# Kernel tuning notes

Measured on AMD Instinct MI355X. Metric: run time of the kernel, lower is better.

Reference implementation:

```python
import jax, jax.numpy as jnp
import numpy as np

L, D, H, F = 2, 512, 8, 2048
B, S = 1, 2048
DH = D // H
EPS = 1e-6
NEG = -1e9


def setup_inputs() -> dict:
    key = jax.random.key(0)
    ks = jax.random.split(key, 8)
    s = 0.02
    return {
        "x": jax.random.normal(ks[0], (B, S, D), jnp.float32),
        "enc_output": jax.random.normal(ks[1], (B, S, D), jnp.float32),
        # per-layer stacked params; axis 1 of attn weights = [wq, wk, wv, wo]
        "attn1_w": jax.random.normal(ks[2], (L, 4, D, D), jnp.float32) * s,
        "attn1_b": jnp.zeros((L, 4, D), jnp.float32),
        "attn2_w": jax.random.normal(ks[3], (L, 4, D, D), jnp.float32) * s,
        "attn2_b": jnp.zeros((L, 4, D), jnp.float32),
        "ffn_w1": jax.random.normal(ks[4], (L, D, F), jnp.float32) * s,
        "ffn_b1": jnp.zeros((L, F), jnp.float32),
        "ffn_w2": jax.random.normal(ks[5], (L, F, D), jnp.float32) * s,
        "ffn_b2": jnp.zeros((L, D), jnp.float32),
        # axis 1 = [norm1, norm2, norm3]
        "ln_g": jnp.ones((L, 3, D), jnp.float32),
        "ln_b": jnp.zeros((L, 3, D), jnp.float32),
    }


def positional_encoding(seq_len, num_feat):
    pos = jnp.arange(seq_len, dtype=jnp.float32)[:, None]
    dims = jnp.arange(num_feat, dtype=jnp.float32)[None, :]
    rates = 1.0 / jnp.power(10000.0, 2.0 * jnp.floor(dims / 2.0) / num_feat)
    ang = pos * rates  # [S, D]
    # keras module concatenates sines(even cols) and cosines(odd cols)
    return jnp.concatenate([jnp.sin(ang[:, 0::2]), jnp.cos(ang[:, 1::2])], axis=-1)[None]


def layer_norm(x, g, b):
    mu = jnp.mean(x, axis=-1, keepdims=True)
    var = jnp.mean(jnp.square(x - mu), axis=-1, keepdims=True)
    return (x - mu) * jax.lax.rsqrt(var + EPS) * g + b


def split_heads(x):
    b, s, _ = x.shape
    return x.reshape(b, s, H, DH).transpose(0, 2, 1, 3)  # [B,H,S,dh]


def mha(q_in, k_in, v_in, w, bias, mask):
    q = split_heads(q_in @ w[0] + bias[0])
    k = split_heads(k_in @ w[1] + bias[1])
    v = split_heads(v_in @ w[2] + bias[2])
    logits = jnp.einsum("bhqd,bhkd->bhqk", q, k) / jnp.sqrt(jnp.float32(DH))
    if mask is not None:
        logits = logits + mask * NEG
    weights = jax.nn.softmax(logits, axis=-1)
    out = jnp.einsum("bhqk,bhkd->bhqd", weights, v)
    b, _, s, _ = out.shape
    out = out.transpose(0, 2, 1, 3).reshape(b, s, D)
    return out @ w[3] + bias[3]


def decoder_forward(x, enc_output, attn1_w, attn1_b, attn2_w, attn2_b,
                    ffn_w1, ffn_b1, ffn_w2, ffn_b2, ln_g, ln_b):
    s = x.shape[1]
    x = x + positional_encoding(s, x.shape[2])
    causal = jnp.triu(jnp.ones((s, s), jnp.float32), k=1)[None, None]  # 1 = masked

    def layer(x, p):
        a1w, a1b, a2w, a2b, w1, b1, w2, b2, g, bn = p
        attn1 = mha(x, x, x, a1w, a1b, causal)
        x = layer_norm(x + attn1, g[0], bn[0])
        attn2 = mha(x, enc_output, enc_output, a2w, a2b, None)
        x = layer_norm(x + attn2, g[1], bn[1])
        ffn = jax.nn.relu(x @ w1 + b1) @ w2 + b2
        x = layer_norm(x + ffn, g[2], bn[2])
        return x, None

    x, _ = jax.lax.scan(layer, x, (attn1_w, attn1_b, attn2_w, attn2_b,
                                   ffn_w1, ffn_b1, ffn_w2, ffn_b2, ln_g, ln_b))
    return x


def reference(x, enc_output, attn1_w, attn1_b, attn2_w, attn2_b,
              ffn_w1, ffn_b1, ffn_w2, ffn_b2, ln_g, ln_b):
    return decoder_forward(x, enc_output, attn1_w, attn1_b, attn2_w, attn2_b,
                           ffn_w1, ffn_b1, ffn_w2, ffn_b2, ln_g, ln_b)
```

## Files before the change

### kernel.cpp

```cpp
#include <hip/hip_runtime.h>
#include <hip/hip_bf16.h>
#include <math.h>

#define S 2048
#define D 512
#define H 8
#define DH 64
#define F 2048
#define NLAYER 2

typedef __attribute__((ext_vector_type(8))) short bf16x8;
typedef __attribute__((ext_vector_type(4))) float f32x4;
typedef __hip_bfloat16 bf16;

typedef __attribute__((address_space(3))) unsigned int lds_u32;
typedef __attribute__((address_space(1))) const unsigned int glb_u32;

__device__ __forceinline__ void gld16(const void* g, void* l) {
    __builtin_amdgcn_global_load_lds((glb_u32*)g, (lds_u32*)l, 16, 0, 0);
}

__global__ void prep_kernel(const float* __restrict__ x, const float* __restrict__ enc,
                            float* __restrict__ xbF, bf16* __restrict__ xbB,
                            bf16* __restrict__ encB) {
    int idx = blockIdx.x * blockDim.x + threadIdx.x;
    if (idx >= S * D) return;
    int s = idx / D;
    int j = idx % D;
    int jj = (j < D / 2) ? j : j - D / 2;
    float rate = expf(-(float)jj * (logf(10000.0f) / (float)(D / 2)));
    float ang = (float)s * rate;
    float pe = (j < D / 2) ? sinf(ang) : cosf(ang);
    float v = x[idx] + pe;
    xbF[idx] = v;
    xbB[idx] = __float2bfloat16(v);
    encB[idx] = __float2bfloat16(enc[idx]);
}

__global__ __launch_bounds__(256)
void transpose_cvt_b(const float* __restrict__ in, bf16* __restrict__ out, int R, int C,
                     size_t inStride, size_t outL, size_t outM, int mpl)
{
    __shared__ float t[64][65];
    const int z = blockIdx.z;
    const float* src = in + (size_t)z * inStride;
    bf16* dst = out + (size_t)(z / mpl) * outL + (size_t)(z % mpl) * outM;
    const int rb = blockIdx.x * 64, cb = blockIdx.y * 64;
    for (int i = threadIdx.x; i < 4096; i += 256) {
        int r = i >> 6, c = i & 63;
        t[r][c] = src[(size_t)(rb + r) * C + cb + c];
    }
    __syncthreads();
    for (int i = threadIdx.x; i < 4096; i += 256) {
        int r = i >> 6, c = i & 63;
        dst[(size_t)(cb + r) * R + rb + c] = __float2bfloat16(t[c][r]);
    }
}

template<int BM, int BN, int BK, int MODE>
__global__ __launch_bounds__(256)
void gemm_bf16(const bf16* __restrict__ A, const bf16* __restrict__ Bt,
               const float* __restrict__ bias, float* __restrict__ outF,
               bf16* __restrict__ outB, int K, int ldc, int relu,
               bf16* __restrict__ q16, bf16* __restrict__ kh,
               bf16* __restrict__ vt, int qn, int kn)
{
    constexpr int MI = BM / 32, NJ = BN / 32;
    constexpr int SL = BK / 8;
    constexpr int KS = BK / 32;
    constexpr int HALF = (BM + BN) * BK * 2;
    constexpr int IA = BM * SL / 256, IB = BN * SL / 256;
    __shared__ char lds[2 * HALF];
    const int tid = threadIdx.x;
    const int w = tid >> 6, l = tid & 63;
    const int l15 = l & 15, l4 = l >> 4;
    const int bm = blockIdx.y * BM, bn = blockIdx.x * BN;
    const int wr = (w >> 1) * (BM / 2), wc = (w & 1) * (BN / 2);

    f32x4 acc[MI][NJ] = {};

#define XV(row) ((BK == 64) ? ((row) & 7) : (((row) >> 1) & 3))
#define GSTAGE(k0, b)                                                          \
    {                                                                          \
        _Pragma("unroll")                                                      \
        for (int i = 0; i < IA; ++i) {                                         \
            int n = (w * IA + i) * 64 + l;                                     \
            int row = n / SL;                                                  \
            int sl = (n % SL) ^ XV(row);                                       \
            gld16(A + (size_t)(bm + row) * K + (k0) + sl * 8,                  \
                  lds + (b) * HALF + (w * IA + i) * 1024);                     \
        }                                                                      \
        _Pragma("unroll")                                                      \
        for (int i = 0; i < IB; ++i) {                                         \
            int n = (w * IB + i) * 64 + l;                                     \
            int row = n / SL;                                                  \
            int sl = (n % SL) ^ XV(row);                                       \
            gld16(Bt + (size_t)(bn + row) * K + (k0) + sl * 8,                 \
                  lds + (b) * HALF + BM * BK * 2 + (w * IB + i) * 1024);       \
        }                                                                      \
    }

    GSTAGE(0, 0);
    __syncthreads();
    int cur = 0;
    for (int k0 = 0; k0 < K; k0 += BK) {
        if (k0 + BK < K) GSTAGE(k0 + BK, cur ^ 1);
        const char* base = lds + cur * HALF;
        bf16x8 af[MI][KS], bfr[NJ][KS];
#pragma unroll
        for (int i = 0; i < MI; ++i) {
            int row = wr + i * 16 + l15;
#pragma unroll
            for (int s = 0; s < KS; ++s)
                af[i][s] = *(const bf16x8*)(base + row * (BK * 2)
                                            + (((s * 4 + l4) ^ XV(row)) << 4));
        }
#pragma unroll
        for (int j = 0; j < NJ; ++j) {
            int row = wc + j * 16 + l15;
#pragma unroll
            for (int s = 0; s < KS; ++s)
                bfr[j][s] = *(const bf16x8*)(base + BM * BK * 2 + row * (BK * 2)
                                             + (((s * 4 + l4) ^ XV(row)) << 4));
        }
#pragma unroll
        for (int s = 0; s < KS; ++s)
#pragma unroll
            for (int i = 0; i < MI; ++i)
#pragma unroll
                for (int j = 0; j < NJ; ++j)
                    acc[i][j] = __builtin_amdgcn_mfma_f32_16x16x32_bf16(af[i][s], bfr[j][s], acc[i][j], 0, 0, 0);
        __syncthreads();
        cur ^= 1;
    }
#undef GSTAGE
#undef XV

    if (MODE == 0) {
#pragma unroll
        for (int i = 0; i < MI; ++i)
#pragma unroll
            for (int j = 0; j < NJ; ++j)
#pragma unroll
                for (int q = 0; q < 4; ++q) {
                    int row = bm + wr + i * 16 + l4 * 4 + q;
                    int col = bn + wc + j * 16 + l15;
                    float v = acc[i][j][q] + bias[col];
                    if (relu) v = fmaxf(v, 0.f);
                    if (outF) outF[(size_t)row * ldc + col] = v;
                    if (outB) outB[(size_t)row * ldc + col] = __float2bfloat16(v);
                }
    } else {
        const int creg = (bn < qn) ? 0 : (bn < qn + kn ? 1 : 2);
        if (creg < 2) {
#pragma unroll
            for (int i = 0; i < MI; ++i)
#pragma unroll
                for (int j = 0; j < NJ; ++j)
#pragma unroll
                    for (int q = 0; q < 4; ++q) {
                        int row = bm + wr + i * 16 + l4 * 4 + q;
                        int col = bn + wc + j * 16 + l15;
                        float v = acc[i][j][q] + bias[col];
                        if (creg == 0) {
                            q16[(size_t)row * 512 + col] = __float2bfloat16(v);
                        } else {
                            int c2 = col - qn;
                            kh[((size_t)(c2 >> 6) * S + row) * 64 + (c2 & 63)] = __float2bfloat16(v);
                        }
                    }
        } else {
            short* t = (short*)lds;
#pragma unroll
            for (int i = 0; i < MI; ++i)
#pragma unroll
                for (int j = 0; j < NJ; ++j)
#pragma unroll
                    for (int q = 0; q < 4; ++q) {
                        int r = wr + i * 16 + l4 * 4 + q;
                        int c = wc + j * 16 + l15;
                        float v = acc[i][j][q] + bias[bn + c];
                        t[r * 72 + c] = __builtin_bit_cast(short, __float2bfloat16(v));
                    }
            __syncthreads();
            const int dgb = bn - qn - kn;
            for (int i2 = tid; i2 < 512; i2 += 256) {
                int dl = i2 >> 3, s8 = (i2 & 7) * 8;
                bf16x8 v;
#pragma unroll
                for (int jj = 0; jj < 8; ++jj)
                    v[jj] = t[(s8 + jj) * 72 + dl];
                *(bf16x8*)(vt + (size_t)(dgb + dl) * S + bm + s8) = v;
            }
        }
    }
}

template<int CAUSAL>
__global__ __launch_bounds__(256)
void attn_mfma6(const bf16* __restrict__ Q, const bf16* __restrict__ Kh,
                const bf16* __restrict__ Vt, bf16* __restrict__ O)
{
    __shared__ char lds[40960];
    const int tid = threadIdx.x;
    const int w = tid >> 6, l = tid & 63;
    const int l15 = l & 15, l4 = l >> 4;
    const int h = blockIdx.x, qb = blockIdx.y;
    const int qw = qb * 64 + w * 16;
    const int qr = qw + l15;
    char* plds = lds + 32768 + w * 2048;

    const float QSC = 0.1803368801f;
    bf16x8 aq[2];
#pragma unroll
    for (int s = 0; s < 2; ++s) {
        bf16x8 raw = *(const bf16x8*)(Q + (size_t)(qw + l15) * 512 + h * DH + s * 32 + l4 * 8);
#pragma unroll
        for (int j = 0; j < 8; ++j) {
            float f = __builtin_bit_cast(float, ((unsigned int)(unsigned short)raw[j]) << 16) * QSC;
            raw[j] = __builtin_bit_cast(short, __float2bfloat16(f));
        }
        aq[s] = raw;
    }

    f32x4 o[4] = {};
    float mrun = -1e30f, lrun = 0.f;
    const int cmax = CAUSAL ? qb : (S / 64 - 1);

#define STAGE(c, b)                                                                 \
    {                                                                               \
        const int kb2 = (c) * 64;                                                   \
        _Pragma("unroll")                                                           \
        for (int i = 0; i < 2; ++i) {                                               \
            int n = w * 128 + i * 64 + l;                                           \
            int row = n >> 3;                                                       \
            int sl = (n & 7) ^ (row & 7);                                           \
            gld16(Kh + ((size_t)h * S + kb2 + row) * 64 + sl * 8,                   \
                  lds + (b) * 16384 + w * 2048 + i * 1024);                         \
            gld16(Vt + ((size_t)(h * 64 + row)) * S + kb2 + sl * 8,                 \
                  lds + (b) * 16384 + 8192 + w * 2048 + i * 1024);                  \
        }                                                                           \
    }

    STAGE(0, 0);
    __syncthreads();

    int cur = 0;
    for (int c = 0; c <= cmax; ++c) {
        if (c < cmax) STAGE(c + 1, cur ^ 1);
        const char* kb = lds + cur * 16384;
        const char* vb = kb + 8192;
        const int kbase = c * 64;

        f32x4 st[4];
#pragma unroll
        for (int t = 0; t < 4; ++t) {
            f32x4 sacc = {0.f, 0.f, 0.f, 0.f};
#pragma unroll
            for (int s = 0; s < 2; ++s) {
                bf16x8 kf = *(const bf16x8*)(kb + (t * 16 + l15) * 128
                                             + (((s * 4 + l4) ^ (l15 & 7)) << 4));
                sacc = __builtin_amdgcn_mfma_f32_16x16x32_bf16(kf, aq[s], sacc, 0, 0, 0);
            }
            st[t] = sacc;
        }

        float mx = -1e30f;
#pragma unroll
        for (int t = 0; t < 4; ++t)
#pragma unroll
            for (int r = 0; r < 4; ++r) {
                float v = st[t][r];
                if (CAUSAL && c == cmax) {
                    int key = kbase + t * 16 + l4 * 4 + r;
                    if (key > qr) v = -1e30f;
                }
                st[t][r] = v;
                mx = fmaxf(mx, v);
            }
        mx = fmaxf(mx, __shfl_xor(mx, 16));
        mx = fmaxf(mx, __shfl_xor(mx, 32));

        if (__any(mx > mrun + 8.0f)) {
            float mnew = fmaxf(mrun, mx);
            float scl = exp2f(mrun - mnew);
            mrun = mnew;
            lrun *= scl;
#pragma unroll
            for (int j = 0; j < 4; ++j) {
                float sj = __shfl(scl, (l & 48) | (l4 * 4 + j));
#pragma unroll
                for (int dt = 0; dt < 4; ++dt) o[dt][j] *= sj;
            }
        }

        float ps = 0.f;
#pragma unroll
        for (int t = 0; t < 4; ++t) {
            float e0 = exp2f(st[t][0] - mrun);
            float e1 = exp2f(st[t][1] - mrun);
            float e2 = exp2f(st[t][2] - mrun);
            float e3 = exp2f(st[t][3] - mrun);
            ps += (e0 + e1) + (e2 + e3);
            unsigned int lo = (unsigned int)(unsigned short)__builtin_bit_cast(short, __float2bfloat16(e0))
                            | ((unsigned int)(unsigned short)__builtin_bit_cast(short, __float2bfloat16(e1)) << 16);
            unsigned int hi = (unsigned int)(unsigned short)__builtin_bit_cast(short, __float2bfloat16(e2))
                            | ((unsigned int)(unsigned short)__builtin_bit_cast(short, __float2bfloat16(e3)) << 16);
            uint2 pk; pk.x = lo; pk.y = hi;
            int byte = (l15 * 128 + t * 32 + l4 * 8) ^ ((l15 & 7) << 4);
            *(uint2*)(plds + byte) = pk;
        }
        ps += __shfl_xor(ps, 16);
        ps += __shfl_xor(ps, 32);
        lrun += ps;

        bf16x8 pf[2];
#pragma unroll
        for (int s = 0; s < 2; ++s) {
            int byte = (l15 * 128 + s * 64 + l4 * 16) ^ ((l15 & 7) << 4);
            pf[s] = *(const bf16x8*)(plds + byte);
        }
#pragma unroll
        for (int dt = 0; dt < 4; ++dt)
#pragma unroll
            for (int s = 0; s < 2; ++s) {
                bf16x8 vf = *(const bf16x8*)(vb + (dt * 16 + l15) * 128
                                             + (((s * 4 + l4) ^ (l15 & 7)) << 4));
                o[dt] = __builtin_amdgcn_mfma_f32_16x16x32_bf16(pf[s], vf, o[dt], 0, 0, 0);
            }

        __syncthreads();
        cur ^= 1;
    }
#undef STAGE

    float linv[4];
#pragma unroll
    for (int j = 0; j < 4; ++j)
        linv[j] = 1.f / __shfl(lrun, (l & 48) | (l4 * 4 + j));
#pragma unroll
    for (int dt = 0; dt < 4; ++dt)
#pragma unroll
        for (int j = 0; j < 4; ++j)
            O[(size_t)(qw + l4 * 4 + j) * D + h * DH + dt * 16 + l15] =
                __float2bfloat16(o[dt][j] * linv[j]);
}

__global__ __launch_bounds__(128)
void add_ln_kernel(const float* __restrict__ a, const float* __restrict__ b,
                   const float* __restrict__ g, const float* __restrict__ beta,
                   float* __restrict__ outF, bf16* __restrict__ outB)
{
    const int row = blockIdx.x;
    const int tid = threadIdx.x;
    float4 av = *(const float4*)&a[(size_t)row * D + tid * 4];
    float4 bv = *(const float4*)&b[(size_t)row * D + tid * 4];
    float4 s;
    s.x = av.x + bv.x; s.y = av.y + bv.y; s.z = av.z + bv.z; s.w = av.w + bv.w;
    float sum = s.x + s.y + s.z + s.w;
    float sq = s.x * s.x + s.y * s.y + s.z * s.z + s.w * s.w;
#pragma unroll
    for (int off = 32; off > 0; off >>= 1) {
        sum += __shfl_xor(sum, off);
        sq  += __shfl_xor(sq, off);
    }
    __shared__ float red[4];
    if ((tid & 63) == 0) { red[(tid >> 6) * 2] = sum; red[(tid >> 6) * 2 + 1] = sq; }
    __syncthreads();
    sum = red[0] + red[2];
    sq  = red[1] + red[3];
    float mu = sum / (float)D;
    float var = sq / (float)D - mu * mu;
    float rs = rsqrtf(var + 1e-6f);
    float4 gv = *(const float4*)&g[tid * 4];
    float4 bt = *(const float4*)&beta[tid * 4];
    float4 o;
    o.x = (s.x - mu) * rs * gv.x + bt.x;
    o.y = (s.y - mu) * rs * gv.y + bt.y;
    o.z = (s.z - mu) * rs * gv.z + bt.z;
    o.w = (s.w - mu) * rs * gv.w + bt.w;
    *(float4*)&outF[(size_t)row * D + tid * 4] = o;
    if (outB) {
        outB[(size_t)row * D + tid * 4 + 0] = __float2bfloat16(o.x);
        outB[(size_t)row * D + tid * 4 + 1] = __float2bfloat16(o.y);
        outB[(size_t)row * D + tid * 4 + 2] = __float2bfloat16(o.z);
        outB[(size_t)row * D + tid * 4 + 3] = __float2bfloat16(o.w);
    }
}

extern "C" void kernel_launch(void* const* d_in, const int* in_sizes, int n_in,
                              void* d_out, int out_size, void* d_ws, size_t ws_size,
                              hipStream_t stream)
{
    const float* x   = (const float*)d_in[0];
    const float* enc = (const float*)d_in[1];
    const float* a1w = (const float*)d_in[2];
    const float* a1b = (const float*)d_in[3];
    const float* a2w = (const float*)d_in[4];
    const float* a2b = (const float*)d_in[5];
    const float* fw1 = (const float*)d_in[6];
    const float* fb1 = (const float*)d_in[7];
    const float* fw2 = (const float*)d_in[8];
    const float* fb2 = (const float*)d_in[9];
    const float* lng = (const float*)d_in[10];
    const float* lnb = (const float*)d_in[11];
    float* out = (float*)d_out;

    char* wsb = (char*)d_ws;
    float* xb   = (float*)(wsb);
    float* ao   = (float*)(wsb + ((size_t)4 << 20));
    bf16* xb16  = (bf16*)(wsb + ((size_t)8 << 20));
    bf16* enc16 = (bf16*)(wsb + ((size_t)10 << 20));
    bf16* att16 = (bf16*)(wsb + ((size_t)12 << 20));
    bf16* q16   = (bf16*)(wsb + ((size_t)14 << 20));
    bf16* kh16  = (bf16*)(wsb + ((size_t)16 << 20));
    bf16* vt16  = (bf16*)(wsb + ((size_t)18 << 20));
    bf16* ffh16 = att16;
    bf16* wts   = (bf16*)(wsb + ((size_t)20 << 20));
    const size_t WCH = 1048576;
    const size_t DD = (size_t)D * D, DF = (size_t)D * F;

    transpose_cvt_b<<<dim3(8, 8, 8), 256, 0, stream>>>(a1w, wts,            D, D, DD, WCH, DD, 4);
    transpose_cvt_b<<<dim3(8, 8, 8), 256, 0, stream>>>(a2w, wts + 2 * WCH,  D, D, DD, WCH, DD, 4);
    transpose_cvt_b<<<dim3(8, 32, 2), 256, 0, stream>>>(fw1, wts + 4 * WCH, D, F, DF, WCH, 0, 1);
    transpose_cvt_b<<<dim3(32, 8, 2), 256, 0, stream>>>(fw2, wts + 6 * WCH, F, D, DF, WCH, 0, 1);
    prep_kernel<<<(S * D + 255) / 256, 256, 0, stream>>>(x, enc, xb, xb16, enc16);

    for (int l = 0; l < NLAYER; ++l) {
        const bf16* A1T = wts + (size_t)(0 + l) * WCH;
        const bf16* A2T = wts + (size_t)(2 + l) * WCH;
        const bf16* W1T = wts + (size_t)(4 + l) * WCH;
        const bf16* W2T = wts + (size_t)(6 + l) * WCH;
        const float* b1v = a1b + (size_t)l * 4 * D;
        const float* b2v = a2b + (size_t)l * 4 * D;

        gemm_bf16<64, 64, 64, 1><<<dim3(24, 32), 256, 0, stream>>>(
            xb16, A1T, b1v, nullptr, nullptr, D, 0, 0, q16, kh16, vt16, 512, 512);
        attn_mfma6<1><<<dim3(H, S / 64), 256, 0, stream>>>(q16, kh16, vt16, att16);
        gemm_bf16<64, 64, 64, 0><<<dim3(8, 32), 256, 0, stream>>>(
            att16, A1T + 3 * DD, b1v + 3 * D, ao, nullptr, D, D, 0, nullptr, nullptr, nullptr, 0, 0);
        add_ln_kernel<<<S, 128, 0, stream>>>(xb, ao, lng + (size_t)(l * 3 + 0) * D, lnb + (size_t)(l * 3 + 0) * D, xb, xb16);

        gemm_bf16<64, 64, 64, 0><<<dim3(8, 32), 256, 0, stream>>>(
            xb16, A2T, b2v, nullptr, q16, D, 512, 0, nullptr, nullptr, nullptr, 0, 0);
        gemm_bf16<64, 64, 64, 1><<<dim3(16, 32), 256, 0, stream>>>(
            enc16, A2T + DD, b2v + D, nullptr, nullptr, D, 0, 0, q16, kh16, vt16, 0, 512);
        attn_mfma6<0><<<dim3(H, S / 64), 256, 0, stream>>>(q16, kh16, vt16, att16);
        gemm_bf16<64, 64, 64, 0><<<dim3(8, 32), 256, 0, stream>>>(
            att16, A2T + 3 * DD, b2v + 3 * D, ao, nullptr, D, D, 0, nullptr, nullptr, nullptr, 0, 0);
        add_ln_kernel<<<S, 128, 0, stream>>>(xb, ao, lng + (size_t)(l * 3 + 1) * D, lnb + (size_t)(l * 3 + 1) * D, xb, xb16);

        gemm_bf16<64, 64, 64, 0><<<dim3(32, 32), 256, 0, stream>>>(
            xb16, W1T, fb1 + (size_t)l * F, nullptr, ffh16, D, F, 1, nullptr, nullptr, nullptr, 0, 0);
        gemm_bf16<64, 64, 64, 0><<<dim3(8, 32), 256, 0, stream>>>(
            ffh16, W2T, fb2 + (size_t)l * D, ao, nullptr, F, D, 0, nullptr, nullptr, nullptr, 0, 0);
        float* dstF = (l == NLAYER - 1) ? out : xb;
        bf16* dstB = (l == NLAYER - 1) ? nullptr : xb16;
        add_ln_kernel<<<S, 128, 0, stream>>>(xb, ao, lng + (size_t)(l * 3 + 2) * D, lnb + (size_t)(l * 3 + 2) * D, dstF, dstB);
    }
}
```

Baseline: 326.8 us.

## Split attention KV loop across two wave groups and enlarge QKV/FFN1 GEMM tiles

The attention kernel now runs 512 threads per block, with two groups of four waves each handling alternate 64-key chunks. Each group keeps its own running max and sum, and the two partial outputs are merged through LDS at the end. This doubles parallelism per query tile and shortens the serial KV loop. Separately, the QKV projections and the first FFN GEMM switch to 128x128x32 tiles, and the V-transpose epilogue is generalised to the larger tile. The changes add LDS use (about 81KB for attention), which lowers occupancy, and the final merge costs an extra bf16 rounding.

```diff
diff --git a/kernel.cpp b/kernel.cpp
--- a/kernel.cpp
+++ b/kernel.cpp
@@ -70,7 +70,10 @@
     constexpr int KS = BK / 32;
     constexpr int HALF = (BM + BN) * BK * 2;
     constexpr int IA = BM * SL / 256, IB = BN * SL / 256;
-    __shared__ char lds[2 * HALF];
+    constexpr int TS = BN + 8;
+    constexpr int LDS_VB = (MODE == 1) ? BM * TS * 2 : 0;
+    constexpr int LDSZ = (2 * HALF > LDS_VB) ? 2 * HALF : LDS_VB;
+    __shared__ char lds[LDSZ];
     const int tid = threadIdx.x;
     const int w = tid >> 6, l = tid & 63;
     const int l15 = l & 15, l4 = l >> 4;
@@ -180,16 +183,18 @@
                         int r = wr + i * 16 + l4 * 4 + q;
                         int c = wc + j * 16 + l15;
                         float v = acc[i][j][q] + bias[bn + c];
-                        t[r * 72 + c] = __builtin_bit_cast(short, __float2bfloat16(v));
+                        t[r * TS + c] = __builtin_bit_cast(short, __float2bfloat16(v));
                     }
             __syncthreads();
             const int dgb = bn - qn - kn;
-            for (int i2 = tid; i2 < 512; i2 += 256) {
-                int dl = i2 >> 3, s8 = (i2 & 7) * 8;
+            constexpr int SGR = BM / 8;
+            for (int i2 = tid; i2 < BN * SGR; i2 += 256) {
+                int dl = i2 / SGR;
+                int s8 = (i2 % SGR) * 8;
                 bf16x8 v;
 #pragma unroll
                 for (int jj = 0; jj < 8; ++jj)
-                    v[jj] = t[(s8 + jj) * 72 + dl];
+                    v[jj] = t[(s8 + jj) * TS + dl];
                 *(bf16x8*)(vt + (size_t)(dgb + dl) * S + bm + s8) = v;
             }
         }
@@ -197,18 +202,19 @@
 }
 
 template<int CAUSAL>
-__global__ __launch_bounds__(256)
-void attn_mfma6(const bf16* __restrict__ Q, const bf16* __restrict__ Kh,
+__global__ __launch_bounds__(512)
+void attn_mfma7(const bf16* __restrict__ Q, const bf16* __restrict__ Kh,
                 const bf16* __restrict__ Vt, bf16* __restrict__ O)
 {
-    __shared__ char lds[40960];
+    __shared__ char lds[82944];
     const int tid = threadIdx.x;
     const int w = tid >> 6, l = tid & 63;
     const int l15 = l & 15, l4 = l >> 4;
+    const int g = w >> 2, wl = w & 3;
     const int h = blockIdx.x, qb = blockIdx.y;
-    const int qw = qb * 64 + w * 16;
+    const int qw = qb * 64 + wl * 16;
     const int qr = qw + l15;
-    char* plds = lds + 32768 + w * 2048;
+    char* plds = lds + 65536 + w * 2048;
 
     const float QSC = 0.1803368801f;
     bf16x8 aq[2];
@@ -226,19 +232,23 @@
     f32x4 o[4] = {};
     float mrun = -1e30f, lrun = 0.f;
     const int cmax = CAUSAL ? qb : (S / 64 - 1);
-
-#define STAGE(c, b)                                                                 \
+    const int nits = cmax / 2 + 1;
+
+#define STAGE(ii, p)                                                                \
     {                                                                               \
-        const int kb2 = (c) * 64;                                                   \
-        _Pragma("unroll")                                                           \
-        for (int i = 0; i < 2; ++i) {                                               \
-            int n = w * 128 + i * 64 + l;                                           \
-            int row = n >> 3;                                                       \
-            int sl = (n & 7) ^ (row & 7);                                           \
-            gld16(Kh + ((size_t)h * S + kb2 + row) * 64 + sl * 8,                   \
-                  lds + (b) * 16384 + w * 2048 + i * 1024);                         \
-            gld16(Vt + ((size_t)(h * 64 + row)) * S + kb2 + sl * 8,                 \
-                  lds + (b) * 16384 + 8192 + w * 2048 + i * 1024);                  \
+        const int cc = 2 * (ii) + g;                                                \
+        if (cc <= cmax) {                                                           \
+            const int kb2 = cc * 64;                                                \
+            _Pragma("unroll")                                                       \
+            for (int i = 0; i < 2; ++i) {                                           \
+                int n = wl * 128 + i * 64 + l;                                      \
+                int row = n >> 3;                                                   \
+                int sl = (n & 7) ^ (row & 7);                                       \
+                gld16(Kh + ((size_t)h * S + kb2 + row) * 64 + sl * 8,               \
+                      lds + (p) * 32768 + g * 16384 + wl * 2048 + i * 1024);        \
+                gld16(Vt + ((size_t)(h * 64 + row)) * S + kb2 + sl * 8,             \
+                      lds + (p) * 32768 + g * 16384 + 8192 + wl * 2048 + i * 1024); \
+            }                                                                       \
         }                                                                           \
     }
 
@@ -246,104 +256,138 @@
     __syncthreads();
 
     int cur = 0;
-    for (int c = 0; c <= cmax; ++c) {
-        if (c < cmax) STAGE(c + 1, cur ^ 1);
-        const char* kb = lds + cur * 16384;
-        const char* vb = kb + 8192;
-        const int kbase = c * 64;
-
-        f32x4 st[4];
-#pragma unroll
-        for (int t = 0; t < 4; ++t) {
-            f32x4 sacc = {0.f, 0.f, 0.f, 0.f};
+    for (int it = 0; it < nits; ++it) {
+        if (it + 1 < nits) STAGE(it + 1, cur ^ 1);
+        const int c = 2 * it + g;
+        if (c <= cmax) {
+            const char* kb = lds + cur * 32768 + g * 16384;
+            const char* vb = kb + 8192;
+            const int kbase = c * 64;
+
+            f32x4 st[4];
+#pragma unroll
+            for (int t = 0; t < 4; ++t) {
+                f32x4 sacc = {0.f, 0.f, 0.f, 0.f};
+#pragma unroll
+                for (int s = 0; s < 2; ++s) {
+                    bf16x8 kf = *(const bf16x8*)(kb + (t * 16 + l15) * 128
+                                                 + (((s * 4 + l4) ^ (l15 & 7)) << 4));
+                    sacc = __builtin_amdgcn_mfma_f32_16x16x32_bf16(kf, aq[s], sacc, 0, 0, 0);
+                }
+                st[t] = sacc;
+            }
+
+            float mx = -1e30f;
+#pragma unroll
+            for (int t = 0; t < 4; ++t)
+#pragma unroll
+                for (int r = 0; r < 4; ++r) {
+                    float v = st[t][r];
+                    if (CAUSAL && c == cmax) {
+                        int key = kbase + t * 16 + l4 * 4 + r;
+                        if (key > qr) v = -1e30f;
+                    }
+                    st[t][r] = v;
+                    mx = fmaxf(mx, v);
+                }
+            mx = fmaxf(mx, __shfl_xor(mx, 16));
+            mx = fmaxf(mx, __shfl_xor(mx, 32));
+
+            if (__any(mx > mrun + 8.0f)) {
+                float mnew = fmaxf(mrun, mx);
+                float scl = exp2f(mrun - mnew);
+                mrun = mnew;
+                lrun *= scl;
+#pragma unroll
+                for (int j = 0; j < 4; ++j) {
+                    float sj = __shfl(scl, (l & 48) | (l4 * 4 + j));
+#pragma unroll
+                    for (int dt = 0; dt < 4; ++dt) o[dt][j] *= sj;
+                }
+            }
+
+            float ps = 0.f;
+#pragma unroll
+            for (int t = 0; t < 4; ++t) {
+                float e0 = exp2f(st[t][0] - mrun);
+                float e1 = exp2f(st[t][1] - mrun);
+                float e2 = exp2f(st[t][2] - mrun);
+                float e3 = exp2f(st[t][3] - mrun);
+                ps += (e0 + e1) + (e2 + e3);
+                unsigned int lo = (unsigned int)(unsigned short)__builtin_bit_cast(short, __float2bfloat16(e0))
+                                | ((unsigned int)(unsigned short)__builtin_bit_cast(short, __float2bfloat16(e1)) << 16);
+                unsigned int hi = (unsigned int)(unsigned short)__builtin_bit_cast(short, __float2bfloat16(e2))
+                                | ((unsigned int)(unsigned short)__builtin_bit_cast(short, __float2bfloat16(e3)) << 16);
+                uint2 pk; pk.x = lo; pk.y = hi;
+                int byte = (l15 * 128 + t * 32 + l4 * 8) ^ ((l15 & 7) << 4);
+                *(uint2*)(plds + byte) = pk;
+            }
+            ps += __shfl_xor(ps, 16);
+            ps += __shfl_xor(ps, 32);
+            lrun += ps;
+
+            bf16x8 pf[2];
 #pragma unroll
             for (int s = 0; s < 2; ++s) {
-                bf16x8 kf = *(const bf16x8*)(kb + (t * 16 + l15) * 128
-                                             + (((s * 4 + l4) ^ (l15 & 7)) << 4));
-                sacc = __builtin_amdgcn_mfma_f32_16x16x32_bf16(kf, aq[s], sacc, 0, 0, 0);
+                int byte = (l15 * 128 + s * 64 + l4 * 16) ^ ((l15 & 7) << 4);
+                pf[s] = *(const bf16x8*)(plds + byte);
             }
-            st[t] = sacc;
-        }
-
-        float mx = -1e30f;
-#pragma unroll
-        for (int t = 0; t < 4; ++t)
-#pragma unroll
-            for (int r = 0; r < 4; ++r) {
-                float v = st[t][r];
-                if (CAUSAL && c == cmax) {
-                    int key = kbase + t * 16 + l4 * 4 + r;
-                    if (key > qr) v = -1e30f;
+#pragma unroll
+            for (int dt = 0; dt < 4; ++dt)
+#pragma unroll
+                for (int s = 0; s < 2; ++s) {
+                    bf16x8 vf = *(const bf16x8*)(vb + (dt * 16 + l15) * 128
+                                                 + (((s * 4 + l4) ^ (l15 & 7)) << 4));
+                    o[dt] = __builtin_amdgcn_mfma_f32_16x16x32_bf16(pf[s], vf, o[dt], 0, 0, 0);
                 }
-                st[t][r] = v;
-                mx = fmaxf(mx, v);
-            }
-        mx = fmaxf(mx, __shfl_xor(mx, 16));
-        mx = fmaxf(mx, __shfl_xor(mx, 32));
-
-        if (__any(mx > mrun + 8.0f)) {
-            float mnew = fmaxf(mrun, mx);
-            float scl = exp2f(mrun - mnew);
-            mrun = mnew;
-            lrun *= scl;
-#pragma unroll
-            for (int j = 0; j < 4; ++j) {
-                float sj = __shfl(scl, (l & 48) | (l4 * 4 + j));
-#pragma unroll
-                for (int dt = 0; dt < 4; ++dt) o[dt][j] *= sj;
-            }
-        }
-
-        float ps = 0.f;
-#pragma unroll
-        for (int t = 0; t < 4; ++t) {
-            float e0 = exp2f(st[t][0] - mrun);
-            float e1 = exp2f(st[t][1] - mrun);
-            float e2 = exp2f(st[t][2] - mrun);
-            float e3 = exp2f(st[t][3] - mrun);
-            ps += (e0 + e1) + (e2 + e3);
-            unsigned int lo = (unsigned int)(unsigned short)__builtin_bit_cast(short, __float2bfloat16(e0))
-                            | ((unsigned int)(unsigned short)__builtin_bit_cast(short, __float2bfloat16(e1)) << 16);
-            unsigned int hi = (unsigned int)(unsigned short)__builtin_bit_cast(short, __float2bfloat16(e2))
-                            | ((unsigned int)(unsigned short)__builtin_bit_cast(short, __float2bfloat16(e3)) << 16);
-            uint2 pk; pk.x = lo; pk.y = hi;
-            int byte = (l15 * 128 + t * 32 + l4 * 8) ^ ((l15 & 7) << 4);
-            *(uint2*)(plds + byte) = pk;
-        }
-        ps += __shfl_xor(ps, 16);
-        ps += __shfl_xor(ps, 32);
-        lrun += ps;
-
-        bf16x8 pf[2];
-#pragma unroll
-        for (int s = 0; s < 2; ++s) {
-            int byte = (l15 * 128 + s * 64 + l4 * 16) ^ ((l15 & 7) << 4);
-            pf[s] = *(const bf16x8*)(plds + byte);
-        }
-#pragma unroll
-        for (int dt = 0; dt < 4; ++dt)
-#pragma unroll
-            for (int s = 0; s < 2; ++s) {
-                bf16x8 vf = *(const bf16x8*)(vb + (dt * 16 + l15) * 128
-                                             + (((s * 4 + l4) ^ (l15 & 7)) << 4));
-                o[dt] = __builtin_amdgcn_mfma_f32_16x16x32_bf16(pf[s], vf, o[dt], 0, 0, 0);
-            }
-
+        }
         __syncthreads();
         cur ^= 1;
     }
 #undef STAGE
 
-    float linv[4];
-#pragma unroll
-    for (int j = 0; j < 4; ++j)
-        linv[j] = 1.f / __shfl(lrun, (l & 48) | (l4 * 4 + j));
 #pragma unroll
     for (int dt = 0; dt < 4; ++dt)
 #pragma unroll
-        for (int j = 0; j < 4; ++j)
-            O[(size_t)(qw + l4 * 4 + j) * D + h * DH + dt * 16 + l15] =
-                __float2bfloat16(o[dt][j] * linv[j]);
+        for (int j = 0; j < 4; ++j) {
+            int q = l4 * 4 + j;
+            int d = dt * 16 + l15;
+            int byte = q * 128 + ((d * 2) ^ ((q & 7) << 4));
+            *(short*)(plds + byte) = __builtin_bit_cast(short, __float2bfloat16(o[dt][j]));
+        }
+    if (l < 16) {
+        *(float*)(lds + 81920 + w * 128 + l * 8) = mrun;
+        *(float*)(lds + 81920 + w * 128 + l * 8 + 4) = lrun;
+    }
+    __syncthreads();
+
+    {
+        const int qt16 = tid >> 7;
+        const int idx = tid & 127;
+        const int q = idx >> 3;
+        const int d0 = (idx & 7) * 8;
+        const char* p0 = lds + 65536 + qt16 * 2048;
+        const char* p1 = lds + 65536 + (qt16 + 4) * 2048;
+        float m0 = *(const float*)(lds + 81920 + qt16 * 128 + q * 8);
+        float l0 = *(const float*)(lds + 81920 + qt16 * 128 + q * 8 + 4);
+        float m1 = *(const float*)(lds + 81920 + (qt16 + 4) * 128 + q * 8);
+        float l1 = *(const float*)(lds + 81920 + (qt16 + 4) * 128 + q * 8 + 4);
+        float mt = fmaxf(m0, m1);
+        float f0 = exp2f(m0 - mt), f1 = exp2f(m1 - mt);
+        float lt = f0 * l0 + f1 * l1;
+        float inv = 1.f / lt;
+        int byte = q * 128 + ((d0 * 2) ^ ((q & 7) << 4));
+        bf16x8 a = *(const bf16x8*)(p0 + byte);
+        bf16x8 b = *(const bf16x8*)(p1 + byte);
+        bf16x8 r;
+#pragma unroll
+        for (int jj = 0; jj < 8; ++jj) {
+            float va = __builtin_bit_cast(float, ((unsigned int)(unsigned short)a[jj]) << 16);
+            float vb2 = __builtin_bit_cast(float, ((unsigned int)(unsigned short)b[jj]) << 16);
+            r[jj] = __builtin_bit_cast(short, __float2bfloat16((f0 * va + f1 * vb2) * inv));
+        }
+        *(bf16x8*)(O + (size_t)(qb * 64 + qt16 * 16 + q) * D + h * DH + d0) = r;
+    }
 }
 
 __global__ __launch_bounds__(128)
@@ -434,23 +478,23 @@
         const float* b1v = a1b + (size_t)l * 4 * D;
         const float* b2v = a2b + (size_t)l * 4 * D;
 
-        gemm_bf16<64, 64, 64, 1><<<dim3(24, 32), 256, 0, stream>>>(
+        gemm_bf16<128, 128, 32, 1><<<dim3(12, 16), 256, 0, stream>>>(
             xb16, A1T, b1v, nullptr, nullptr, D, 0, 0, q16, kh16, vt16, 512, 512);
-        attn_mfma6<1><<<dim3(H, S / 64), 256, 0, stream>>>(q16, kh16, vt16, att16);
+        attn_mfma7<1><<<dim3(H, S / 64), 512, 0, stream>>>(q16, kh16, vt16, att16);
         gemm_bf16<64, 64, 64, 0><<<dim3(8, 32), 256, 0, stream>>>(
             att16, A1T + 3 * DD, b1v + 3 * D, ao, nullptr, D, D, 0, nullptr, nullptr, nullptr, 0, 0);
         add_ln_kernel<<<S, 128, 0, stream>>>(xb, ao, lng + (size_t)(l * 3 + 0) * D, lnb + (size_t)(l * 3 + 0) * D, xb, xb16);
 
         gemm_bf16<64, 64, 64, 0><<<dim3(8, 32), 256, 0, stream>>>(
             xb16, A2T, b2v, nullptr, q16, D, 512, 0, nullptr, nullptr, nullptr, 0, 0);
-        gemm_bf16<64, 64, 64, 1><<<dim3(16, 32), 256, 0, stream>>>(
+        gemm_bf16<128, 128, 32, 1><<<dim3(8, 16), 256, 0, stream>>>(
             enc16, A2T + DD, b2v + D, nullptr, nullptr, D, 0, 0, q16, kh16, vt16, 0, 512);
-        attn_mfma6<0><<<dim3(H, S / 64), 256, 0, stream>>>(q16, kh16, vt16, att16);
+        attn_mfma7<0><<<dim3(H, S / 64), 512, 0, stream>>>(q16, kh16, vt16, att16);
         gemm_bf16<64, 64, 64, 0><<<dim3(8, 32), 256, 0, stream>>>(
             att16, A2T + 3 * DD, b2v + 3 * D, ao, nullptr, D, D, 0, nullptr, nullptr, nullptr, 0, 0);
         add_ln_kernel<<<S, 128, 0, stream>>>(xb, ao, lng + (size_t)(l * 3 + 1) * D, lnb + (size_t)(l * 3 + 1) * D, xb, xb16);
 
-        gemm_bf16<64, 64, 64, 0><<<dim3(32, 32), 256, 0, stream>>>(
+        gemm_bf16<128, 128, 32, 0><<<dim3(16, 16), 256, 0, stream>>>(
             xb16, W1T, fb1 + (size_t)l * F, nullptr, ffh16, D, F, 1, nullptr, nullptr, nullptr, 0, 0);
         gemm_bf16<64, 64, 64, 0><<<dim3(8, 32), 256, 0, stream>>>(
             ffh16, W2T, fb2 + (size_t)l * D, ao, nullptr, F, D, 0, nullptr, nullptr, nullptr, 0, 0);
```

Result: no change. 331.0 us (+1.3%).
